# Kernel tuning notes

Measured on AMD Instinct MI355X. Metric: run time of the kernel, lower is better.

## Reference

```python
import jax, jax.numpy as jnp
import numpy as np

SEQ_LEN = 96
D_MODEL = 512
BATCH = 512
FREQ = SEQ_LEN // 2 + 1  # 49
EPS = 1e-5


def setup_inputs() -> dict:
    key = jax.random.key(0)
    ks = jax.random.split(key, 9)
    s = 1.0 / np.sqrt(D_MODEL)
    return {
        "x": jax.random.normal(ks[0], (BATCH, SEQ_LEN, D_MODEL), jnp.float32),
        "freq_weights": jnp.ones((FREQ,), jnp.float32),
        "Wl": jax.random.normal(ks[1], (D_MODEL, D_MODEL), jnp.float32) * s,
        "bl": jax.random.normal(ks[2], (D_MODEL,), jnp.float32) * s,
        "Wh": jax.random.normal(ks[3], (D_MODEL, D_MODEL), jnp.float32) * s,
        "bh": jax.random.normal(ks[4], (D_MODEL,), jnp.float32) * s,
        "Wg": jax.random.normal(ks[5], (2 * D_MODEL, D_MODEL), jnp.float32) * s,
        "bg": jax.random.normal(ks[6], (D_MODEL,), jnp.float32) * s,
        "gamma": jnp.ones((D_MODEL,), jnp.float32),
        "beta": jnp.zeros((D_MODEL,), jnp.float32),
    }


def reference(x, freq_weights, Wl, bl, Wh, bh, Wg, bg, gamma, beta):
    # Batched rfft over seq axis for all channels at once: [B, F, D] complex
    xf = jnp.fft.rfft(x, axis=1)
    xw = xf * freq_weights[None, :, None]
    cutoff = FREQ // 3  # 16 (static)
    idx = jnp.arange(FREQ)[None, :, None]
    x_low_f = jnp.where(idx < cutoff, xw, 0)
    x_high_f = jnp.where(idx >= cutoff, xw, 0)
    x_low = jnp.fft.irfft(x_low_f, n=SEQ_LEN, axis=1)   # [B, S, D]
    x_high = jnp.fft.irfft(x_high_f, n=SEQ_LEN, axis=1)
    x_low = jnp.einsum("bsd,de->bse", x_low, Wl) + bl
    x_high = jnp.einsum("bsd,de->bse", x_high, Wh) + bh
    gate_in = jnp.concatenate([x_low, x_high], axis=-1)  # [B, S, 2D]
    gate = jax.nn.sigmoid(jnp.einsum("bsd,de->bse", gate_in, Wg) + bg)
    out = gate * x_low + (1.0 - gate) * x_high
    y = x + out  # dropout is identity in eval mode
    mu = jnp.mean(y, axis=-1, keepdims=True)
    var = jnp.var(y, axis=-1, keepdims=True)
    return (y - mu) / jnp.sqrt(var + EPS) * gamma + beta
```

## Files before the change

kernel.cpp:

```cpp
#include <hip/hip_runtime.h>

typedef unsigned short u16;
typedef unsigned int u32;

#define SEQ 96
#define DM 512
#define NBATCH 512
#define NFREQ 49
#define CUT 16
#define MROWS (NBATCH * SEQ)

typedef __attribute__((ext_vector_type(8))) short bf16x8;
typedef __attribute__((ext_vector_type(4))) float f32x4;

__device__ __forceinline__ u16 f2bf(float f) {
  u32 u = __float_as_uint(f);
  u32 r = (u + 0x7fffu + ((u >> 16) & 1u)) >> 16;
  return (u16)r;
}
__device__ __forceinline__ float bf2f(u16 u) {
  return __uint_as_float(((u32)u) << 16);
}

__device__ __forceinline__ void g2l16(const void* g, void* l) {
  __builtin_amdgcn_global_load_lds(
      (const __attribute__((address_space(1))) void*)g,
      (__attribute__((address_space(3))) void*)l, 16, 0, 0);
}

__global__ void build_filters_k(const float* __restrict__ w,
                                u16* __restrict__ FlB, u16* __restrict__ FhB) {
  int idx = blockIdx.x * 256 + threadIdx.x;
  if (idx >= SEQ * SEQ) return;
  int s = idx / SEQ, t = idx % SEQ;
  int d = s - t;
  const float scale = 1.0f / (float)SEQ;
  const float w0 = 6.283185307179586f / (float)SEQ;
  float cl = 0.f, ch = 0.f;
  for (int k = 0; k < NFREQ; k++) {
    int m = (k * d) % SEQ;
    if (m < 0) m += SEQ;
    float c = (k == 0 || k == SEQ / 2) ? 1.0f : 2.0f;
    float v = c * w[k] * cosf(w0 * (float)m) * scale;
    if (k < CUT) cl += v; else ch += v;
  }
  FlB[idx] = f2bf(cl);
  FhB[idx] = f2bf(ch);
}

__global__ void __launch_bounds__(256) transpose_w_k(
    const float* __restrict__ W, u16* __restrict__ Wt, int K, int N) {
  __shared__ float t[32][33];
  int k0 = blockIdx.x * 32, n0 = blockIdx.y * 32;
  int tx = threadIdx.x & 31, ty = threadIdx.x >> 5;
  #pragma unroll
  for (int r = 0; r < 32; r += 8)
    t[ty + r][tx] = W[(size_t)(k0 + ty + r) * N + n0 + tx];
  __syncthreads();
  #pragma unroll
  for (int r = 0; r < 32; r += 8)
    Wt[(size_t)(n0 + ty + r) * K + k0 + tx] = f2bf(t[tx][ty + r]);
}

__global__ void __launch_bounds__(256) xt_k(
    const float* __restrict__ x, u16* __restrict__ xT) {
  __shared__ float xs[SEQ * 65];
  int b = blockIdx.x;
  int d0 = blockIdx.y * 64;
  const float* xb = x + (size_t)b * SEQ * DM + d0;
  #pragma unroll
  for (int v = 0; v < 6; v++) {
    int c = v * 256 + threadIdx.x;
    int t = c >> 4, dq = (c & 15) << 2;
    float4 f = *(const float4*)(xb + (size_t)t * DM + dq);
    xs[t * 65 + dq + 0] = f.x;
    xs[t * 65 + dq + 1] = f.y;
    xs[t * 65 + dq + 2] = f.z;
    xs[t * 65 + dq + 3] = f.w;
  }
  __syncthreads();
  u32* outw = (u32*)(xT + ((size_t)b * DM + d0) * SEQ);
  #pragma unroll
  for (int v = 0; v < 12; v++) {
    int c = v * 256 + threadIdx.x;
    int d = c / 48, tw = c % 48;
    int t0 = tw * 2;
    u32 lo = (u32)f2bf(xs[t0 * 65 + d]);
    u32 hi = (u32)f2bf(xs[(t0 + 1) * 65 + d]);
    outw[(size_t)d * 48 + tw] = lo | (hi << 16);
  }
}

__global__ void __launch_bounds__(256) filter_mfma_k(
    const u16* __restrict__ xT, const u16* __restrict__ FlB,
    const u16* __restrict__ FhB, u16* __restrict__ xl, u16* __restrict__ xh) {
  __shared__ __align__(16) u16 lds[128 * SEQ + 2 * SEQ * SEQ];
  u16* Bs = lds;
  u16* As0 = lds + 128 * SEQ;
  int tid = threadIdx.x;
  int lane = tid & 63, w = tid >> 6;
  int b = blockIdx.x, d0 = blockIdx.y * 128;

  const u16* xbase = xT + ((size_t)b * DM + d0) * SEQ;
  #pragma unroll
  for (int it = 0; it < 6; it++) {
    int c = it * 256 + tid;
    int row = c / 12, off = (c % 12) * 8;
    g2l16(xbase + (size_t)row * SEQ + off, (char*)Bs + (((it * 256 + w * 64)) << 4));
  }
  #pragma unroll
  for (int it = 0; it < 9; it++) {
    int c = it * 256 + tid;
    const u16* src = (c < 1152) ? (FlB + c * 8) : (FhB + (c - 1152) * 8);
    g2l16(src, (char*)As0 + ((it * 256 + w * 64) << 4));
  }
  __syncthreads();

  const int l15 = lane & 15, lq = lane >> 4;
  f32x4 acc[2][6][2] = {};
  #pragma unroll
  for (int ks = 0; ks < 3; ks++) {
    int kt = ks * 32;
    bf16x8 bf[2];
    #pragma unroll
    for (int j = 0; j < 2; j++)
      bf[j] = *(const bf16x8*)&Bs[(w * 32 + j * 16 + l15) * SEQ + kt + lq * 8];
    #pragma unroll
    for (int f = 0; f < 2; f++)
      #pragma unroll
      for (int i = 0; i < 6; i++) {
        bf16x8 af = *(const bf16x8*)&As0[f * SEQ * SEQ + (i * 16 + l15) * SEQ + kt + lq * 8];
        #pragma unroll
        for (int j = 0; j < 2; j++)
          acc[f][i][j] = __builtin_amdgcn_mfma_f32_16x16x32_bf16(af, bf[j], acc[f][i][j], 0, 0, 0);
      }
  }
  #pragma unroll
  for (int f = 0; f < 2; f++) {
    u16* dst = f ? xh : xl;
    #pragma unroll
    for (int i = 0; i < 6; i++)
      #pragma unroll
      for (int j = 0; j < 2; j++) {
        int d = d0 + w * 32 + j * 16 + l15;
        #pragma unroll
        for (int r = 0; r < 4; r++) {
          int s = i * 16 + lq * 4 + r;
          dst[((size_t)b * SEQ + s) * DM + d] = f2bf(acc[f][i][j][r]);
        }
      }
  }
}

__global__ void __launch_bounds__(256) gemm_proj_mfma_k(
    const u16* __restrict__ xl, const u16* __restrict__ xh,
    const u16* __restrict__ Wlt, const u16* __restrict__ Wht,
    const float* __restrict__ bl, const float* __restrict__ bh,
    u16* __restrict__ yl, u16* __restrict__ yh) {
  const u16* A = blockIdx.z ? xh : xl;
  const u16* Bt = blockIdx.z ? Wht : Wlt;
  const float* bias = blockIdx.z ? bh : bl;
  u16* C = blockIdx.z ? yh : yl;

  __shared__ __align__(16) u16 As[128 * 32];
  __shared__ __align__(16) u16 Bs[128 * 32];
  const int m0 = blockIdx.x * 128;
  const int n0 = blockIdx.y * 128;
  const int tid = threadIdx.x;
  const int lane = tid & 63;
  const int w = tid >> 6;
  const int wm = w & 1, wn = w >> 1;
  const int l15 = lane & 15;
  const int lq = lane >> 4;

  f32x4 acc[4][4] = {};

  for (int kt = 0; kt < 512; kt += 32) {
    #pragma unroll
    for (int r = 0; r < 2; r++) {
      int chunk = r * 256 + tid;
      int row = chunk >> 2;
      int ce = (chunk & 3) << 3;
      u32 lo = (u32)((r * 256 + w * 64) << 4);
      g2l16(A + (size_t)(m0 + row) * 512 + kt + ce, (char*)As + lo);
      g2l16(Bt + (size_t)(n0 + row) * 512 + kt + ce, (char*)Bs + lo);
    }
    __syncthreads();
    bf16x8 af[4], bf[4];
    #pragma unroll
    for (int i = 0; i < 4; i++)
      af[i] = *(const bf16x8*)&As[(wm * 64 + i * 16 + l15) * 32 + lq * 8];
    #pragma unroll
    for (int j = 0; j < 4; j++)
      bf[j] = *(const bf16x8*)&Bs[(wn * 64 + j * 16 + l15) * 32 + lq * 8];
    #pragma unroll
    for (int i = 0; i < 4; i++)
      #pragma unroll
      for (int j = 0; j < 4; j++)
        acc[i][j] = __builtin_amdgcn_mfma_f32_16x16x32_bf16(af[i], bf[j], acc[i][j], 0, 0, 0);
    __syncthreads();
  }

  #pragma unroll
  for (int j = 0; j < 4; j++) {
    int n = n0 + wn * 64 + j * 16 + l15;
    float bv = bias[n];
    #pragma unroll
    for (int i = 0; i < 4; i++) {
      int mrow = m0 + wm * 64 + i * 16 + lq * 4;
      #pragma unroll
      for (int r = 0; r < 4; r++)
        C[(size_t)(mrow + r) * 512 + n] = f2bf(acc[i][j][r] + bv);
    }
  }
}

__global__ void __launch_bounds__(256) gemm_gate_mfma_k(
    const u16* __restrict__ yl, const u16* __restrict__ yh,
    const u16* __restrict__ Wgt, const float* __restrict__ bg,
    u16* __restrict__ g) {
  __shared__ __align__(16) u16 As[128 * 32];
  __shared__ __align__(16) u16 Bs[128 * 32];
  const int m0 = blockIdx.x * 128;
  const int n0 = blockIdx.y * 128;
  const int tid = threadIdx.x;
  const int lane = tid & 63;
  const int w = tid >> 6;
  const int wm = w & 1, wn = w >> 1;
  const int l15 = lane & 15;
  const int lq = lane >> 4;

  f32x4 acc[4][4] = {};

  for (int kt = 0; kt < 1024; kt += 32) {
    const u16* Ak = (kt < 512) ? yl : yh;
    int ka = kt & 511;
    #pragma unroll
    for (int r = 0; r < 2; r++) {
      int chunk = r * 256 + tid;
      int row = chunk >> 2;
      int ce = (chunk & 3) << 3;
      u32 lo = (u32)((r * 256 + w * 64) << 4);
      g2l16(Ak + (size_t)(m0 + row) * 512 + ka + ce, (char*)As + lo);
      g2l16(Wgt + (size_t)(n0 + row) * 1024 + kt + ce, (char*)Bs + lo);
    }
    __syncthreads();
    bf16x8 af[4], bf[4];
    #pragma unroll
    for (int i = 0; i < 4; i++)
      af[i] = *(const bf16x8*)&As[(wm * 64 + i * 16 + l15) * 32 + lq * 8];
    #pragma unroll
    for (int j = 0; j < 4; j++)
      bf[j] = *(const bf16x8*)&Bs[(wn * 64 + j * 16 + l15) * 32 + lq * 8];
    #pragma unroll
    for (int i = 0; i < 4; i++)
      #pragma unroll
      for (int j = 0; j < 4; j++)
        acc[i][j] = __builtin_amdgcn_mfma_f32_16x16x32_bf16(af[i], bf[j], acc[i][j], 0, 0, 0);
    __syncthreads();
  }

  #pragma unroll
  for (int j = 0; j < 4; j++) {
    int n = n0 + wn * 64 + j * 16 + l15;
    float bv = bg[n];
    #pragma unroll
    for (int i = 0; i < 4; i++) {
      int mrow = m0 + wm * 64 + i * 16 + lq * 4;
      #pragma unroll
      for (int r = 0; r < 4; r++) {
        float z = acc[i][j][r] + bv;
        g[(size_t)(mrow + r) * 512 + n] = f2bf(1.0f / (1.0f + __expf(-z)));
      }
    }
  }
}

__global__ void __launch_bounds__(256) final_ln_k(
    const float* __restrict__ x, const u16* __restrict__ yl,
    const u16* __restrict__ yh, const u16* __restrict__ g,
    const float* __restrict__ gamma, const float* __restrict__ beta,
    float* __restrict__ out) {
  __shared__ float red[8];
  int r = blockIdx.x;
  size_t base = (size_t)r * 512;
  float vv[2];
  float sum = 0.f, sumsq = 0.f;
  #pragma unroll
  for (int j = 0; j < 2; j++) {
    int e = threadIdx.x + j * 256;
    float lv = bf2f(yl[base + e]);
    float hv = bf2f(yh[base + e]);
    float gv = bf2f(g[base + e]);
    float v = x[base + e] + gv * lv + (1.f - gv) * hv;
    vv[j] = v;
    sum += v;
    sumsq += v * v;
  }
  #pragma unroll
  for (int off = 32; off; off >>= 1) {
    sum += __shfl_down(sum, off);
    sumsq += __shfl_down(sumsq, off);
  }
  int wid = threadIdx.x >> 6;
  if ((threadIdx.x & 63) == 0) {
    red[wid] = sum;
    red[4 + wid] = sumsq;
  }
  __syncthreads();
  sum = red[0] + red[1] + red[2] + red[3];
  sumsq = red[4] + red[5] + red[6] + red[7];
  float mu = sum * (1.f / 512.f);
  float var = sumsq * (1.f / 512.f) - mu * mu;
  float inv = rsqrtf(var + 1e-5f);
  #pragma unroll
  for (int j = 0; j < 2; j++) {
    int e = threadIdx.x + j * 256;
    out[base + e] = (vv[j] - mu) * inv * gamma[e] + beta[e];
  }
}

extern "C" void kernel_launch(void* const* d_in, const int* in_sizes, int n_in,
                              void* d_out, int out_size, void* d_ws, size_t ws_size,
                              hipStream_t stream) {
  const float* x     = (const float*)d_in[0];
  const float* fw    = (const float*)d_in[1];
  const float* Wl    = (const float*)d_in[2];
  const float* bl    = (const float*)d_in[3];
  const float* Wh    = (const float*)d_in[4];
  const float* bh    = (const float*)d_in[5];
  const float* Wg    = (const float*)d_in[6];
  const float* bg    = (const float*)d_in[7];
  const float* gamma = (const float*)d_in[8];
  const float* beta  = (const float*)d_in[9];
  float* out = (float*)d_out;

  char* ws = (char*)d_ws;
  u16* FlB = (u16*)ws;
  u16* FhB = FlB + SEQ * SEQ;
  u16* Wlt = (u16*)(ws + 64 * 1024);
  u16* Wht = Wlt + 512 * 512;
  u16* Wgt = Wht + 512 * 512;
  size_t tsz = (size_t)MROWS * 512;
  u16* xl = (u16*)(ws + 4 * 1024 * 1024);
  u16* xh = xl + tsz;
  u16* yl = xh + tsz;
  u16* yh = yl + tsz;
  u16* xT = yl;
  u16* gbuf = xl;

  build_filters_k<<<dim3(36), dim3(256), 0, stream>>>(fw, FlB, FhB);
  transpose_w_k<<<dim3(16, 16), dim3(256), 0, stream>>>(Wl, Wlt, 512, 512);
  transpose_w_k<<<dim3(16, 16), dim3(256), 0, stream>>>(Wh, Wht, 512, 512);
  transpose_w_k<<<dim3(32, 16), dim3(256), 0, stream>>>(Wg, Wgt, 1024, 512);
  xt_k<<<dim3(NBATCH, DM / 64), dim3(256), 0, stream>>>(x, xT);
  filter_mfma_k<<<dim3(NBATCH, DM / 128), dim3(256), 0, stream>>>(xT, FlB, FhB, xl, xh);
  gemm_proj_mfma_k<<<dim3(MROWS / 128, 4, 2), dim3(256), 0, stream>>>(
      xl, xh, Wlt, Wht, bl, bh, yl, yh);
  gemm_gate_mfma_k<<<dim3(MROWS / 128, 4), dim3(256), 0, stream>>>(yl, yh, Wgt, bg, gbuf);
  final_ln_k<<<dim3(MROWS), dim3(256), 0, stream>>>(x, yl, yh, gbuf, gamma, beta, out);
}
```

Baseline: 467.6 us.

## Fuse projection GEMMs, gate GEMM and LayerNorm into one row-block kernel

Replaces the two projection GEMMs, the gate GEMM and the LayerNorm kernel with a single kernel. Each block owns 64 rows and all 512 output columns, keeps the projected low/high activations in swizzled shared memory, and runs the gate GEMM and LayerNorm epilogue on-chip. This removes the global round-trips of the yl/yh/gate intermediates and three launches. In exchange, A/B fragments are loaded straight from global memory with register double-buffering instead of an LDS-staged tile. There is also less weight reuse per block, and the large shared footprint (128KB for Y) may limit occupancy.

```diff
diff --git a/kernel.cpp b/kernel.cpp
--- a/kernel.cpp
+++ b/kernel.cpp
@@ -9,6 +9,7 @@
 #define NFREQ 49
 #define CUT 16
 #define MROWS (NBATCH * SEQ)
+#define MBLK 64
 
 typedef __attribute__((ext_vector_type(8))) short bf16x8;
 typedef __attribute__((ext_vector_type(4))) float f32x4;
@@ -121,18 +122,18 @@
   #pragma unroll
   for (int ks = 0; ks < 3; ks++) {
     int kt = ks * 32;
-    bf16x8 bf[2];
+    bf16x8 bfr[2];
     #pragma unroll
     for (int j = 0; j < 2; j++)
-      bf[j] = *(const bf16x8*)&Bs[(w * 32 + j * 16 + l15) * SEQ + kt + lq * 8];
+      bfr[j] = *(const bf16x8*)&Bs[(w * 32 + j * 16 + l15) * SEQ + kt + lq * 8];
     #pragma unroll
     for (int f = 0; f < 2; f++)
       #pragma unroll
       for (int i = 0; i < 6; i++) {
-        bf16x8 af = *(const bf16x8*)&As0[f * SEQ * SEQ + (i * 16 + l15) * SEQ + kt + lq * 8];
+        bf16x8 afr = *(const bf16x8*)&As0[f * SEQ * SEQ + (i * 16 + l15) * SEQ + kt + lq * 8];
         #pragma unroll
         for (int j = 0; j < 2; j++)
-          acc[f][i][j] = __builtin_amdgcn_mfma_f32_16x16x32_bf16(af, bf[j], acc[f][i][j], 0, 0, 0);
+          acc[f][i][j] = __builtin_amdgcn_mfma_f32_16x16x32_bf16(afr, bfr[j], acc[f][i][j], 0, 0, 0);
       }
   }
   #pragma unroll
@@ -152,171 +153,184 @@
   }
 }
 
-__global__ void __launch_bounds__(256) gemm_proj_mfma_k(
+__global__ void __launch_bounds__(512, 2) mega_k(
     const u16* __restrict__ xl, const u16* __restrict__ xh,
     const u16* __restrict__ Wlt, const u16* __restrict__ Wht,
+    const u16* __restrict__ Wgt,
     const float* __restrict__ bl, const float* __restrict__ bh,
-    u16* __restrict__ yl, u16* __restrict__ yh) {
-  const u16* A = blockIdx.z ? xh : xl;
-  const u16* Bt = blockIdx.z ? Wht : Wlt;
-  const float* bias = blockIdx.z ? bh : bl;
-  u16* C = blockIdx.z ? yh : yl;
-
-  __shared__ __align__(16) u16 As[128 * 32];
-  __shared__ __align__(16) u16 Bs[128 * 32];
-  const int m0 = blockIdx.x * 128;
-  const int n0 = blockIdx.y * 128;
+    const float* __restrict__ bg, const float* __restrict__ x,
+    const float* __restrict__ gamma, const float* __restrict__ beta,
+    float* __restrict__ out) {
+  __shared__ __align__(16) u16 Y[2][MBLK][DM];
+  __shared__ float redS[MBLK][8];
+  __shared__ float redQ[MBLK][8];
+  __shared__ float musd[MBLK][2];
+
   const int tid = threadIdx.x;
   const int lane = tid & 63;
   const int w = tid >> 6;
-  const int wm = w & 1, wn = w >> 1;
   const int l15 = lane & 15;
   const int lq = lane >> 4;
-
-  f32x4 acc[4][4] = {};
-
-  for (int kt = 0; kt < 512; kt += 32) {
-    #pragma unroll
-    for (int r = 0; r < 2; r++) {
-      int chunk = r * 256 + tid;
-      int row = chunk >> 2;
-      int ce = (chunk & 3) << 3;
-      u32 lo = (u32)((r * 256 + w * 64) << 4);
-      g2l16(A + (size_t)(m0 + row) * 512 + kt + ce, (char*)As + lo);
-      g2l16(Bt + (size_t)(n0 + row) * 512 + kt + ce, (char*)Bs + lo);
-    }
-    __syncthreads();
-    bf16x8 af[4], bf[4];
-    #pragma unroll
-    for (int i = 0; i < 4; i++)
-      af[i] = *(const bf16x8*)&As[(wm * 64 + i * 16 + l15) * 32 + lq * 8];
-    #pragma unroll
-    for (int j = 0; j < 4; j++)
-      bf[j] = *(const bf16x8*)&Bs[(wn * 64 + j * 16 + l15) * 32 + lq * 8];
-    #pragma unroll
-    for (int i = 0; i < 4; i++)
-      #pragma unroll
-      for (int j = 0; j < 4; j++)
-        acc[i][j] = __builtin_amdgcn_mfma_f32_16x16x32_bf16(af[i], bf[j], acc[i][j], 0, 0, 0);
-    __syncthreads();
-  }
-
-  #pragma unroll
-  for (int j = 0; j < 4; j++) {
-    int n = n0 + wn * 64 + j * 16 + l15;
-    float bv = bias[n];
-    #pragma unroll
-    for (int i = 0; i < 4; i++) {
-      int mrow = m0 + wm * 64 + i * 16 + lq * 4;
-      #pragma unroll
-      for (int r = 0; r < 4; r++)
-        C[(size_t)(mrow + r) * 512 + n] = f2bf(acc[i][j][r] + bv);
-    }
-  }
-}
-
-__global__ void __launch_bounds__(256) gemm_gate_mfma_k(
-    const u16* __restrict__ yl, const u16* __restrict__ yh,
-    const u16* __restrict__ Wgt, const float* __restrict__ bg,
-    u16* __restrict__ g) {
-  __shared__ __align__(16) u16 As[128 * 32];
-  __shared__ __align__(16) u16 Bs[128 * 32];
-  const int m0 = blockIdx.x * 128;
-  const int n0 = blockIdx.y * 128;
-  const int tid = threadIdx.x;
-  const int lane = tid & 63;
-  const int w = tid >> 6;
-  const int wm = w & 1, wn = w >> 1;
-  const int l15 = lane & 15;
-  const int lq = lane >> 4;
-
-  f32x4 acc[4][4] = {};
-
+  const int m0 = blockIdx.x * MBLK;
+
+  f32x4 acc[4][4];
+  bf16x8 af[2][4], bf[2][4];
+  const f32x4 fzero = {0.f, 0.f, 0.f, 0.f};
+
+  for (int f = 0; f < 2; ++f) {
+    const u16* Ag = f ? xh : xl;
+    const u16* Bg = f ? Wht : Wlt;
+    const float* bias = f ? bh : bl;
+    #pragma unroll
+    for (int i = 0; i < 4; ++i)
+      #pragma unroll
+      for (int j = 0; j < 4; ++j) acc[i][j] = fzero;
+
+    #pragma unroll
+    for (int i = 0; i < 4; ++i)
+      af[0][i] = *(const bf16x8*)&Ag[(size_t)(m0 + i * 16 + l15) * DM + lq * 8];
+    #pragma unroll
+    for (int j = 0; j < 4; ++j)
+      bf[0][j] = *(const bf16x8*)&Bg[(size_t)(w * 64 + j * 16 + l15) * DM + lq * 8];
+
+    #pragma unroll
+    for (int kt = 0; kt < DM; kt += 32) {
+      const int cb = (kt >> 5) & 1, nb = cb ^ 1;
+      if (kt + 32 < DM) {
+        #pragma unroll
+        for (int i = 0; i < 4; ++i)
+          af[nb][i] = *(const bf16x8*)&Ag[(size_t)(m0 + i * 16 + l15) * DM + kt + 32 + lq * 8];
+        #pragma unroll
+        for (int j = 0; j < 4; ++j)
+          bf[nb][j] = *(const bf16x8*)&Bg[(size_t)(w * 64 + j * 16 + l15) * DM + kt + 32 + lq * 8];
+      }
+      #pragma unroll
+      for (int i = 0; i < 4; ++i)
+        #pragma unroll
+        for (int j = 0; j < 4; ++j)
+          acc[i][j] = __builtin_amdgcn_mfma_f32_16x16x32_bf16(af[cb][i], bf[cb][j], acc[i][j], 0, 0, 0);
+    }
+
+    #pragma unroll
+    for (int j = 0; j < 4; ++j) {
+      const int n = w * 64 + j * 16 + l15;
+      const float bv = bias[n];
+      #pragma unroll
+      for (int i = 0; i < 4; ++i)
+        #pragma unroll
+        for (int r = 0; r < 4; ++r) {
+          const int m = i * 16 + lq * 4 + r;
+          Y[f][m][n ^ ((m & 7) << 3)] = f2bf(acc[i][j][r] + bv);
+        }
+    }
+  }
+  __syncthreads();
+
+  #pragma unroll
+  for (int i = 0; i < 4; ++i)
+    #pragma unroll
+    for (int j = 0; j < 4; ++j) acc[i][j] = fzero;
+
+  #pragma unroll
+  for (int i = 0; i < 4; ++i) {
+    const int row = i * 16 + l15;
+    af[0][i] = *(const bf16x8*)&Y[0][row][(lq * 8) ^ ((row & 7) << 3)];
+  }
+  #pragma unroll
+  for (int j = 0; j < 4; ++j)
+    bf[0][j] = *(const bf16x8*)&Wgt[(size_t)(w * 64 + j * 16 + l15) * 1024 + lq * 8];
+
+  #pragma unroll
   for (int kt = 0; kt < 1024; kt += 32) {
-    const u16* Ak = (kt < 512) ? yl : yh;
-    int ka = kt & 511;
-    #pragma unroll
-    for (int r = 0; r < 2; r++) {
-      int chunk = r * 256 + tid;
-      int row = chunk >> 2;
-      int ce = (chunk & 3) << 3;
-      u32 lo = (u32)((r * 256 + w * 64) << 4);
-      g2l16(Ak + (size_t)(m0 + row) * 512 + ka + ce, (char*)As + lo);
-      g2l16(Wgt + (size_t)(n0 + row) * 1024 + kt + ce, (char*)Bs + lo);
-    }
-    __syncthreads();
-    bf16x8 af[4], bf[4];
-    #pragma unroll
-    for (int i = 0; i < 4; i++)
-      af[i] = *(const bf16x8*)&As[(wm * 64 + i * 16 + l15) * 32 + lq * 8];
-    #pragma unroll
-    for (int j = 0; j < 4; j++)
-      bf[j] = *(const bf16x8*)&Bs[(wn * 64 + j * 16 + l15) * 32 + lq * 8];
-    #pragma unroll
-    for (int i = 0; i < 4; i++)
-      #pragma unroll
-      for (int j = 0; j < 4; j++)
-        acc[i][j] = __builtin_amdgcn_mfma_f32_16x16x32_bf16(af[i], bf[j], acc[i][j], 0, 0, 0);
-    __syncthreads();
-  }
-
-  #pragma unroll
-  for (int j = 0; j < 4; j++) {
-    int n = n0 + wn * 64 + j * 16 + l15;
-    float bv = bg[n];
-    #pragma unroll
-    for (int i = 0; i < 4; i++) {
-      int mrow = m0 + wm * 64 + i * 16 + lq * 4;
-      #pragma unroll
-      for (int r = 0; r < 4; r++) {
-        float z = acc[i][j][r] + bv;
-        g[(size_t)(mrow + r) * 512 + n] = f2bf(1.0f / (1.0f + __expf(-z)));
-      }
-    }
-  }
-}
-
-__global__ void __launch_bounds__(256) final_ln_k(
-    const float* __restrict__ x, const u16* __restrict__ yl,
-    const u16* __restrict__ yh, const u16* __restrict__ g,
-    const float* __restrict__ gamma, const float* __restrict__ beta,
-    float* __restrict__ out) {
-  __shared__ float red[8];
-  int r = blockIdx.x;
-  size_t base = (size_t)r * 512;
-  float vv[2];
-  float sum = 0.f, sumsq = 0.f;
-  #pragma unroll
-  for (int j = 0; j < 2; j++) {
-    int e = threadIdx.x + j * 256;
-    float lv = bf2f(yl[base + e]);
-    float hv = bf2f(yh[base + e]);
-    float gv = bf2f(g[base + e]);
-    float v = x[base + e] + gv * lv + (1.f - gv) * hv;
-    vv[j] = v;
-    sum += v;
-    sumsq += v * v;
-  }
-  #pragma unroll
-  for (int off = 32; off; off >>= 1) {
-    sum += __shfl_down(sum, off);
-    sumsq += __shfl_down(sumsq, off);
-  }
-  int wid = threadIdx.x >> 6;
-  if ((threadIdx.x & 63) == 0) {
-    red[wid] = sum;
-    red[4 + wid] = sumsq;
-  }
-  __syncthreads();
-  sum = red[0] + red[1] + red[2] + red[3];
-  sumsq = red[4] + red[5] + red[6] + red[7];
-  float mu = sum * (1.f / 512.f);
-  float var = sumsq * (1.f / 512.f) - mu * mu;
-  float inv = rsqrtf(var + 1e-5f);
-  #pragma unroll
-  for (int j = 0; j < 2; j++) {
-    int e = threadIdx.x + j * 256;
-    out[base + e] = (vv[j] - mu) * inv * gamma[e] + beta[e];
+    const int cb = (kt >> 5) & 1, nb = cb ^ 1;
+    if (kt + 32 < 1024) {
+      const int fn = (kt + 32) >> 9, ka = (kt + 32) & 511;
+      #pragma unroll
+      for (int i = 0; i < 4; ++i) {
+        const int row = i * 16 + l15;
+        af[nb][i] = *(const bf16x8*)&Y[fn][row][(ka + lq * 8) ^ ((row & 7) << 3)];
+      }
+      #pragma unroll
+      for (int j = 0; j < 4; ++j)
+        bf[nb][j] = *(const bf16x8*)&Wgt[(size_t)(w * 64 + j * 16 + l15) * 1024 + kt + 32 + lq * 8];
+    }
+    #pragma unroll
+    for (int i = 0; i < 4; ++i)
+      #pragma unroll
+      for (int j = 0; j < 4; ++j)
+        acc[i][j] = __builtin_amdgcn_mfma_f32_16x16x32_bf16(af[cb][i], bf[cb][j], acc[i][j], 0, 0, 0);
+  }
+
+  #pragma unroll
+  for (int j = 0; j < 4; ++j) {
+    const int n = w * 64 + j * 16 + l15;
+    const float bgv = bg[n];
+    #pragma unroll
+    for (int i = 0; i < 4; ++i)
+      #pragma unroll
+      for (int r = 0; r < 4; ++r) {
+        const int m = i * 16 + lq * 4 + r;
+        const int ns = n ^ ((m & 7) << 3);
+        const float z = acc[i][j][r] + bgv;
+        const float gv = 1.f / (1.f + __expf(-z));
+        const float lv = bf2f(Y[0][m][ns]);
+        const float hv = bf2f(Y[1][m][ns]);
+        acc[i][j][r] = x[(size_t)(m0 + m) * DM + n] + gv * lv + (1.f - gv) * hv;
+      }
+  }
+
+  #pragma unroll
+  for (int i = 0; i < 4; ++i)
+    #pragma unroll
+    for (int r = 0; r < 4; ++r) {
+      float s = 0.f, q = 0.f;
+      #pragma unroll
+      for (int j = 0; j < 4; ++j) {
+        const float v = acc[i][j][r];
+        s += v; q += v * v;
+      }
+      #pragma unroll
+      for (int off = 8; off; off >>= 1) {
+        s += __shfl_xor(s, off);
+        q += __shfl_xor(q, off);
+      }
+      if (l15 == 0) {
+        const int m = i * 16 + lq * 4 + r;
+        redS[m][w] = s;
+        redQ[m][w] = q;
+      }
+    }
+  __syncthreads();
+
+  {
+    const int m = tid >> 3, k = tid & 7;
+    float s = redS[m][k], q = redQ[m][k];
+    #pragma unroll
+    for (int off = 4; off; off >>= 1) {
+      s += __shfl_xor(s, off);
+      q += __shfl_xor(q, off);
+    }
+    if (k == 0) {
+      const float mu = s * (1.f / 512.f);
+      const float var = q * (1.f / 512.f) - mu * mu;
+      musd[m][0] = mu;
+      musd[m][1] = rsqrtf(var + 1e-5f);
+    }
+  }
+  __syncthreads();
+
+  #pragma unroll
+  for (int j = 0; j < 4; ++j) {
+    const int n = w * 64 + j * 16 + l15;
+    const float gm = gamma[n], bt = beta[n];
+    #pragma unroll
+    for (int i = 0; i < 4; ++i)
+      #pragma unroll
+      for (int r = 0; r < 4; ++r) {
+        const int m = i * 16 + lq * 4 + r;
+        const float mu = musd[m][0], inv = musd[m][1];
+        out[(size_t)(m0 + m) * DM + n] = (acc[i][j][r] - mu) * inv * gm + bt;
+      }
   }
 }
 
@@ -344,10 +358,7 @@
   size_t tsz = (size_t)MROWS * 512;
   u16* xl = (u16*)(ws + 4 * 1024 * 1024);
   u16* xh = xl + tsz;
-  u16* yl = xh + tsz;
-  u16* yh = yl + tsz;
-  u16* xT = yl;
-  u16* gbuf = xl;
+  u16* xT = xh + tsz;
 
   build_filters_k<<<dim3(36), dim3(256), 0, stream>>>(fw, FlB, FhB);
   transpose_w_k<<<dim3(16, 16), dim3(256), 0, stream>>>(Wl, Wlt, 512, 512);
@@ -355,8 +366,6 @@
   transpose_w_k<<<dim3(32, 16), dim3(256), 0, stream>>>(Wg, Wgt, 1024, 512);
   xt_k<<<dim3(NBATCH, DM / 64), dim3(256), 0, stream>>>(x, xT);
   filter_mfma_k<<<dim3(NBATCH, DM / 128), dim3(256), 0, stream>>>(xT, FlB, FhB, xl, xh);
-  gemm_proj_mfma_k<<<dim3(MROWS / 128, 4, 2), dim3(256), 0, stream>>>(
-      xl, xh, Wlt, Wht, bl, bh, yl, yh);
-  gemm_gate_mfma_k<<<dim3(MROWS / 128, 4), dim3(256), 0, stream>>>(yl, yh, Wgt, bg, gbuf);
-  final_ln_k<<<dim3(MROWS), dim3(256), 0, stream>>>(x, yl, yh, gbuf, gamma, beta, out);
-}
+  mega_k<<<dim3(MROWS / MBLK), dim3(512), 0, stream>>>(
+      xl, xh, Wlt, Wht, Wgt, bl, bh, bg, x, gamma, beta, out);
+}
```

Result: slower. 574.7 us (+22.9%).

## Fuse x transpose into filter kernel and double-buffer GEMM LDS staging

Applied to the files above, without the earlier changes.

Removes the separate xt_k pass by having the filter kernel read fp32 x directly, transpose it through a small padded LDS tile in four chunks and convert it to bf16 in place. This drops a full write and read of the transposed bf16 intermediate. Both projection GEMMs switch to two LDS stages, issuing the next K-tile's async loads before computing the current one so load latency overlaps MFMA work. The cost is more LDS per block, which can lower occupancy, plus extra barriers inside the filter kernel.

```diff
diff --git a/kernel.cpp b/kernel.cpp
--- a/kernel.cpp
+++ b/kernel.cpp
@@ -62,77 +62,66 @@
     Wt[(size_t)(n0 + ty + r) * K + k0 + tx] = f2bf(t[tx][ty + r]);
 }
 
-__global__ void __launch_bounds__(256) xt_k(
-    const float* __restrict__ x, u16* __restrict__ xT) {
-  __shared__ float xs[SEQ * 65];
-  int b = blockIdx.x;
-  int d0 = blockIdx.y * 64;
-  const float* xb = x + (size_t)b * SEQ * DM + d0;
-  #pragma unroll
-  for (int v = 0; v < 6; v++) {
-    int c = v * 256 + threadIdx.x;
-    int t = c >> 4, dq = (c & 15) << 2;
-    float4 f = *(const float4*)(xb + (size_t)t * DM + dq);
-    xs[t * 65 + dq + 0] = f.x;
-    xs[t * 65 + dq + 1] = f.y;
-    xs[t * 65 + dq + 2] = f.z;
-    xs[t * 65 + dq + 3] = f.w;
-  }
-  __syncthreads();
-  u32* outw = (u32*)(xT + ((size_t)b * DM + d0) * SEQ);
-  #pragma unroll
-  for (int v = 0; v < 12; v++) {
-    int c = v * 256 + threadIdx.x;
-    int d = c / 48, tw = c % 48;
-    int t0 = tw * 2;
-    u32 lo = (u32)f2bf(xs[t0 * 65 + d]);
-    u32 hi = (u32)f2bf(xs[(t0 + 1) * 65 + d]);
-    outw[(size_t)d * 48 + tw] = lo | (hi << 16);
-  }
-}
-
-__global__ void __launch_bounds__(256) filter_mfma_k(
-    const u16* __restrict__ xT, const u16* __restrict__ FlB,
+__global__ void __launch_bounds__(256) filter_fused_k(
+    const float* __restrict__ x, const u16* __restrict__ FlB,
     const u16* __restrict__ FhB, u16* __restrict__ xl, u16* __restrict__ xh) {
-  __shared__ __align__(16) u16 lds[128 * SEQ + 2 * SEQ * SEQ];
-  u16* Bs = lds;
-  u16* As0 = lds + 128 * SEQ;
+  __shared__ __align__(16) u16 Bs[128 * SEQ];
+  __shared__ __align__(16) u16 As0[2 * SEQ * SEQ];
+  __shared__ float xs[SEQ * 33];
   int tid = threadIdx.x;
   int lane = tid & 63, w = tid >> 6;
   int b = blockIdx.x, d0 = blockIdx.y * 128;
 
-  const u16* xbase = xT + ((size_t)b * DM + d0) * SEQ;
-  #pragma unroll
-  for (int it = 0; it < 6; it++) {
-    int c = it * 256 + tid;
-    int row = c / 12, off = (c % 12) * 8;
-    g2l16(xbase + (size_t)row * SEQ + off, (char*)Bs + (((it * 256 + w * 64)) << 4));
-  }
   #pragma unroll
   for (int it = 0; it < 9; it++) {
     int c = it * 256 + tid;
     const u16* src = (c < 1152) ? (FlB + c * 8) : (FhB + (c - 1152) * 8);
     g2l16(src, (char*)As0 + ((it * 256 + w * 64) << 4));
   }
-  __syncthreads();
+
+  const float* xb = x + (size_t)b * SEQ * DM + d0;
+  u32* BsW = (u32*)Bs;
+  #pragma unroll
+  for (int q = 0; q < 4; q++) {
+    #pragma unroll
+    for (int v = 0; v < 3; v++) {
+      int c = v * 256 + tid;
+      int t = c >> 3, f = (c & 7) << 2;
+      float4 fv = *(const float4*)(xb + (size_t)t * DM + q * 32 + f);
+      xs[t * 33 + f + 0] = fv.x;
+      xs[t * 33 + f + 1] = fv.y;
+      xs[t * 33 + f + 2] = fv.z;
+      xs[t * 33 + f + 3] = fv.w;
+    }
+    __syncthreads();
+    #pragma unroll
+    for (int v = 0; v < 6; v++) {
+      int c = v * 256 + tid;
+      int dl = c / 48, tw = c % 48;
+      u32 lo = (u32)f2bf(xs[(2 * tw) * 33 + dl]);
+      u32 hi = (u32)f2bf(xs[(2 * tw + 1) * 33 + dl]);
+      BsW[(size_t)(q * 32 + dl) * 48 + tw] = lo | (hi << 16);
+    }
+    __syncthreads();
+  }
 
   const int l15 = lane & 15, lq = lane >> 4;
   f32x4 acc[2][6][2] = {};
   #pragma unroll
   for (int ks = 0; ks < 3; ks++) {
     int kt = ks * 32;
-    bf16x8 bf[2];
+    bf16x8 bfr[2];
     #pragma unroll
     for (int j = 0; j < 2; j++)
-      bf[j] = *(const bf16x8*)&Bs[(w * 32 + j * 16 + l15) * SEQ + kt + lq * 8];
+      bfr[j] = *(const bf16x8*)&Bs[(w * 32 + j * 16 + l15) * SEQ + kt + lq * 8];
     #pragma unroll
     for (int f = 0; f < 2; f++)
       #pragma unroll
       for (int i = 0; i < 6; i++) {
-        bf16x8 af = *(const bf16x8*)&As0[f * SEQ * SEQ + (i * 16 + l15) * SEQ + kt + lq * 8];
+        bf16x8 afr = *(const bf16x8*)&As0[f * SEQ * SEQ + (i * 16 + l15) * SEQ + kt + lq * 8];
         #pragma unroll
         for (int j = 0; j < 2; j++)
-          acc[f][i][j] = __builtin_amdgcn_mfma_f32_16x16x32_bf16(af, bf[j], acc[f][i][j], 0, 0, 0);
+          acc[f][i][j] = __builtin_amdgcn_mfma_f32_16x16x32_bf16(afr, bfr[j], acc[f][i][j], 0, 0, 0);
       }
   }
   #pragma unroll
@@ -162,8 +151,7 @@
   const float* bias = blockIdx.z ? bh : bl;
   u16* C = blockIdx.z ? yh : yl;
 
-  __shared__ __align__(16) u16 As[128 * 32];
-  __shared__ __align__(16) u16 Bs[128 * 32];
+  __shared__ __align__(16) char stg[2][16384];
   const int m0 = blockIdx.x * 128;
   const int n0 = blockIdx.y * 128;
   const int tid = threadIdx.x;
@@ -175,17 +163,28 @@
 
   f32x4 acc[4][4] = {};
 
-  for (int kt = 0; kt < 512; kt += 32) {
-    #pragma unroll
-    for (int r = 0; r < 2; r++) {
-      int chunk = r * 256 + tid;
-      int row = chunk >> 2;
-      int ce = (chunk & 3) << 3;
-      u32 lo = (u32)((r * 256 + w * 64) << 4);
-      g2l16(A + (size_t)(m0 + row) * 512 + kt + ce, (char*)As + lo);
-      g2l16(Bt + (size_t)(n0 + row) * 512 + kt + ce, (char*)Bs + lo);
-    }
-    __syncthreads();
+  auto stage = [&](int b, int ks) {
+    const int kt = ks * 32;
+    #pragma unroll
+    for (int it = 0; it < 4; it++) {
+      int c = it * 256 + tid;
+      int row = (c & 511) >> 2, ce = (c & 3) << 3;
+      const u16* src = (c < 512)
+          ? A  + (size_t)(m0 + row) * 512 + kt + ce
+          : Bt + (size_t)(n0 + row) * 512 + kt + ce;
+      g2l16(src, stg[b] + ((it * 256 + w * 64) << 4));
+    }
+  };
+
+  stage(0, 0);
+  __syncthreads();
+
+  #pragma unroll 2
+  for (int ks = 0; ks < 16; ks++) {
+    const int cur = ks & 1;
+    if (ks < 15) stage(cur ^ 1, ks + 1);
+    const u16* As = (const u16*)stg[cur];
+    const u16* Bs = As + 4096;
     bf16x8 af[4], bf[4];
     #pragma unroll
     for (int i = 0; i < 4; i++)
@@ -219,8 +218,7 @@
     const u16* __restrict__ yl, const u16* __restrict__ yh,
     const u16* __restrict__ Wgt, const float* __restrict__ bg,
     u16* __restrict__ g) {
-  __shared__ __align__(16) u16 As[128 * 32];
-  __shared__ __align__(16) u16 Bs[128 * 32];
+  __shared__ __align__(16) char stg[2][16384];
   const int m0 = blockIdx.x * 128;
   const int n0 = blockIdx.y * 128;
   const int tid = threadIdx.x;
@@ -230,21 +228,32 @@
   const int l15 = lane & 15;
   const int lq = lane >> 4;
 
+  auto stage = [&](int b, int ks) {
+    const int kt = ks * 32;
+    const int ka = kt & 511;
+    const u16* Ak = (ks < 16) ? yl : yh;
+    #pragma unroll
+    for (int it = 0; it < 4; it++) {
+      int c = it * 256 + tid;
+      int row = (c & 511) >> 2, ce = (c & 3) << 3;
+      const u16* src = (c < 512)
+          ? Ak  + (size_t)(m0 + row) * 512 + ka + ce
+          : Wgt + (size_t)(n0 + row) * 1024 + kt + ce;
+      g2l16(src, stg[b] + ((it * 256 + w * 64) << 4));
+    }
+  };
+
   f32x4 acc[4][4] = {};
 
-  for (int kt = 0; kt < 1024; kt += 32) {
-    const u16* Ak = (kt < 512) ? yl : yh;
-    int ka = kt & 511;
-    #pragma unroll
-    for (int r = 0; r < 2; r++) {
-      int chunk = r * 256 + tid;
-      int row = chunk >> 2;
-      int ce = (chunk & 3) << 3;
-      u32 lo = (u32)((r * 256 + w * 64) << 4);
-      g2l16(Ak + (size_t)(m0 + row) * 512 + ka + ce, (char*)As + lo);
-      g2l16(Wgt + (size_t)(n0 + row) * 1024 + kt + ce, (char*)Bs + lo);
-    }
-    __syncthreads();
+  stage(0, 0);
+  __syncthreads();
+
+  #pragma unroll 2
+  for (int ks = 0; ks < 32; ks++) {
+    const int cur = ks & 1;
+    if (ks < 31) stage(cur ^ 1, ks + 1);
+    const u16* As = (const u16*)stg[cur];
+    const u16* Bs = As + 4096;
     bf16x8 af[4], bf[4];
     #pragma unroll
     for (int i = 0; i < 4; i++)
@@ -346,15 +355,13 @@
   u16* xh = xl + tsz;
   u16* yl = xh + tsz;
   u16* yh = yl + tsz;
-  u16* xT = yl;
   u16* gbuf = xl;
 
   build_filters_k<<<dim3(36), dim3(256), 0, stream>>>(fw, FlB, FhB);
   transpose_w_k<<<dim3(16, 16), dim3(256), 0, stream>>>(Wl, Wlt, 512, 512);
   transpose_w_k<<<dim3(16, 16), dim3(256), 0, stream>>>(Wh, Wht, 512, 512);
   transpose_w_k<<<dim3(32, 16), dim3(256), 0, stream>>>(Wg, Wgt, 1024, 512);
-  xt_k<<<dim3(NBATCH, DM / 64), dim3(256), 0, stream>>>(x, xT);
-  filter_mfma_k<<<dim3(NBATCH, DM / 128), dim3(256), 0, stream>>>(xT, FlB, FhB, xl, xh);
+  filter_fused_k<<<dim3(NBATCH, DM / 128), dim3(256), 0, stream>>>(x, FlB, FhB, xl, xh);
   gemm_proj_mfma_k<<<dim3(MROWS / 128, 4, 2), dim3(256), 0, stream>>>(
       xl, xh, Wlt, Wht, bl, bh, yl, yh);
   gemm_gate_mfma_k<<<dim3(MROWS / 128, 4), dim3(256), 0, stream>>>(yl, yh, Wgt, bg, gbuf);
```

Result: faster. 439.6 us (-6.0%).

## Fuse x transpose into filter kernel and stage outputs through LDS

Applied to the files above, without the earlier changes.

Removes the separate xt_k kernel and its bf16 xT intermediate. The filter kernel now reads fp32 x directly, transposes it in four 32-column chunks through LDS into the B tile, and reads the filter matrices straight from global memory instead of staging them in LDS. Results are written to LDS first and then stored as coalesced 32-bit rows, replacing the previous strided 16-bit global stores. This saves one full write and read of the activation tensor, at the cost of extra barriers and uncached-in-LDS filter loads during the MFMA loop.

```diff
diff --git a/kernel.cpp b/kernel.cpp
--- a/kernel.cpp
+++ b/kernel.cpp
@@ -62,79 +62,67 @@
     Wt[(size_t)(n0 + ty + r) * K + k0 + tx] = f2bf(t[tx][ty + r]);
 }
 
-__global__ void __launch_bounds__(256) xt_k(
-    const float* __restrict__ x, u16* __restrict__ xT) {
-  __shared__ float xs[SEQ * 65];
-  int b = blockIdx.x;
-  int d0 = blockIdx.y * 64;
-  const float* xb = x + (size_t)b * SEQ * DM + d0;
-  #pragma unroll
-  for (int v = 0; v < 6; v++) {
-    int c = v * 256 + threadIdx.x;
-    int t = c >> 4, dq = (c & 15) << 2;
-    float4 f = *(const float4*)(xb + (size_t)t * DM + dq);
-    xs[t * 65 + dq + 0] = f.x;
-    xs[t * 65 + dq + 1] = f.y;
-    xs[t * 65 + dq + 2] = f.z;
-    xs[t * 65 + dq + 3] = f.w;
-  }
-  __syncthreads();
-  u32* outw = (u32*)(xT + ((size_t)b * DM + d0) * SEQ);
-  #pragma unroll
-  for (int v = 0; v < 12; v++) {
-    int c = v * 256 + threadIdx.x;
-    int d = c / 48, tw = c % 48;
-    int t0 = tw * 2;
-    u32 lo = (u32)f2bf(xs[t0 * 65 + d]);
-    u32 hi = (u32)f2bf(xs[(t0 + 1) * 65 + d]);
-    outw[(size_t)d * 48 + tw] = lo | (hi << 16);
-  }
-}
-
-__global__ void __launch_bounds__(256) filter_mfma_k(
-    const u16* __restrict__ xT, const u16* __restrict__ FlB,
+__global__ void __launch_bounds__(256) filter_fused_k(
+    const float* __restrict__ x, const u16* __restrict__ FlB,
     const u16* __restrict__ FhB, u16* __restrict__ xl, u16* __restrict__ xh) {
-  __shared__ __align__(16) u16 lds[128 * SEQ + 2 * SEQ * SEQ];
-  u16* Bs = lds;
-  u16* As0 = lds + 128 * SEQ;
+  __shared__ __align__(16) char ldsbuf[24576 + 12672];
+  u16* Bs = (u16*)ldsbuf;
+  float* xs = (float*)(ldsbuf + 24576);
   int tid = threadIdx.x;
   int lane = tid & 63, w = tid >> 6;
   int b = blockIdx.x, d0 = blockIdx.y * 128;
 
-  const u16* xbase = xT + ((size_t)b * DM + d0) * SEQ;
-  #pragma unroll
-  for (int it = 0; it < 6; it++) {
-    int c = it * 256 + tid;
-    int row = c / 12, off = (c % 12) * 8;
-    g2l16(xbase + (size_t)row * SEQ + off, (char*)Bs + (((it * 256 + w * 64)) << 4));
-  }
-  #pragma unroll
-  for (int it = 0; it < 9; it++) {
-    int c = it * 256 + tid;
-    const u16* src = (c < 1152) ? (FlB + c * 8) : (FhB + (c - 1152) * 8);
-    g2l16(src, (char*)As0 + ((it * 256 + w * 64) << 4));
-  }
-  __syncthreads();
+  const float* xb = x + (size_t)b * SEQ * DM + d0;
+  u32* BsW = (u32*)Bs;
+  #pragma unroll
+  for (int q = 0; q < 4; q++) {
+    #pragma unroll
+    for (int v = 0; v < 3; v++) {
+      int c = v * 256 + tid;
+      int t = c >> 3, f = (c & 7) << 2;
+      float4 fv = *(const float4*)(xb + (size_t)t * DM + q * 32 + f);
+      xs[t * 33 + f + 0] = fv.x;
+      xs[t * 33 + f + 1] = fv.y;
+      xs[t * 33 + f + 2] = fv.z;
+      xs[t * 33 + f + 3] = fv.w;
+    }
+    __syncthreads();
+    #pragma unroll
+    for (int v = 0; v < 6; v++) {
+      int c = v * 256 + tid;
+      int dl = c / 48, tw = c % 48;
+      u32 lo = (u32)f2bf(xs[(2 * tw) * 33 + dl]);
+      u32 hi = (u32)f2bf(xs[(2 * tw + 1) * 33 + dl]);
+      BsW[(size_t)(q * 32 + dl) * 48 + tw] = lo | (hi << 16);
+    }
+    __syncthreads();
+  }
 
   const int l15 = lane & 15, lq = lane >> 4;
   f32x4 acc[2][6][2] = {};
   #pragma unroll
   for (int ks = 0; ks < 3; ks++) {
     int kt = ks * 32;
-    bf16x8 bf[2];
+    bf16x8 bfr[2];
     #pragma unroll
     for (int j = 0; j < 2; j++)
-      bf[j] = *(const bf16x8*)&Bs[(w * 32 + j * 16 + l15) * SEQ + kt + lq * 8];
-    #pragma unroll
-    for (int f = 0; f < 2; f++)
+      bfr[j] = *(const bf16x8*)&Bs[(w * 32 + j * 16 + l15) * SEQ + kt + lq * 8];
+    #pragma unroll
+    for (int f = 0; f < 2; f++) {
+      const u16* Fg = f ? FhB : FlB;
       #pragma unroll
       for (int i = 0; i < 6; i++) {
-        bf16x8 af = *(const bf16x8*)&As0[f * SEQ * SEQ + (i * 16 + l15) * SEQ + kt + lq * 8];
+        bf16x8 afr = *(const bf16x8*)&Fg[(i * 16 + l15) * SEQ + kt + lq * 8];
         #pragma unroll
         for (int j = 0; j < 2; j++)
-          acc[f][i][j] = __builtin_amdgcn_mfma_f32_16x16x32_bf16(af, bf[j], acc[f][i][j], 0, 0, 0);
+          acc[f][i][j] = __builtin_amdgcn_mfma_f32_16x16x32_bf16(afr, bfr[j], acc[f][i][j], 0, 0, 0);
       }
-  }
+    }
+  }
+  __syncthreads();
+
+  u16* T = (u16*)ldsbuf;
+  u32* Tw = (u32*)ldsbuf;
   #pragma unroll
   for (int f = 0; f < 2; f++) {
     u16* dst = f ? xh : xl;
@@ -142,13 +130,22 @@
     for (int i = 0; i < 6; i++)
       #pragma unroll
       for (int j = 0; j < 2; j++) {
-        int d = d0 + w * 32 + j * 16 + l15;
+        int d = w * 32 + j * 16 + l15;
         #pragma unroll
         for (int r = 0; r < 4; r++) {
           int s = i * 16 + lq * 4 + r;
-          dst[((size_t)b * SEQ + s) * DM + d] = f2bf(acc[f][i][j][r]);
+          T[s * 130 + d] = f2bf(acc[f][i][j][r]);
         }
       }
+    __syncthreads();
+    u32* outw = (u32*)(dst + (size_t)b * SEQ * DM + d0);
+    #pragma unroll
+    for (int v = 0; v < 24; v++) {
+      int c = v * 256 + tid;
+      int s = c >> 6, dp = c & 63;
+      outw[s * 256 + dp] = Tw[s * 65 + dp];
+    }
+    __syncthreads();
   }
 }
 
@@ -346,15 +343,13 @@
   u16* xh = xl + tsz;
   u16* yl = xh + tsz;
   u16* yh = yl + tsz;
-  u16* xT = yl;
   u16* gbuf = xl;
 
   build_filters_k<<<dim3(36), dim3(256), 0, stream>>>(fw, FlB, FhB);
   transpose_w_k<<<dim3(16, 16), dim3(256), 0, stream>>>(Wl, Wlt, 512, 512);
   transpose_w_k<<<dim3(16, 16), dim3(256), 0, stream>>>(Wh, Wht, 512, 512);
   transpose_w_k<<<dim3(32, 16), dim3(256), 0, stream>>>(Wg, Wgt, 1024, 512);
-  xt_k<<<dim3(NBATCH, DM / 64), dim3(256), 0, stream>>>(x, xT);
-  filter_mfma_k<<<dim3(NBATCH, DM / 128), dim3(256), 0, stream>>>(xT, FlB, FhB, xl, xh);
+  filter_fused_k<<<dim3(NBATCH, DM / 128), dim3(256), 0, stream>>>(x, FlB, FhB, xl, xh);
   gemm_proj_mfma_k<<<dim3(MROWS / 128, 4, 2), dim3(256), 0, stream>>>(
       xl, xh, Wlt, Wht, bl, bh, yl, yh);
   gemm_gate_mfma_k<<<dim3(MROWS / 128, 4), dim3(256), 0, stream>>>(yl, yh, Wgt, bg, gbuf);
```

Result: faster. 454.5 us (-2.8%).
